# Kernel tuning notes

Hardware: AMD Instinct MI355X
Metric: run time of the kernel (lower is better)

Reference implementation:

```python
import jax, jax.numpy as jnp
import numpy as np

N_QUBITS = 4
LAYERS = 2
NUM_HEADS = 8
EMBED = 32
DK = EMBED // NUM_HEADS  # == N_QUBITS
B, S = 32, 4096


def _ry(t):
    c, s = jnp.cos(t / 2), jnp.sin(t / 2)
    m = jnp.stack([jnp.stack([c, -s], -1), jnp.stack([s, c], -1)], -2)
    return m.astype(jnp.complex64)


def _rx(t):
    c = jnp.cos(t / 2).astype(jnp.complex64)
    s = (-1j) * jnp.sin(t / 2).astype(jnp.complex64)
    return jnp.stack([jnp.stack([c, s], -1), jnp.stack([s, c], -1)], -2)


def _rz(t):
    em = jnp.exp(-0.5j * t.astype(jnp.complex64))
    ep = jnp.conj(em)
    z = jnp.zeros_like(em)
    return jnp.stack([jnp.stack([em, z], -1), jnp.stack([z, ep], -1)], -2)


def _apply_1q(state, U, w, n):
    # state: (B, 2**n); wire 0 is the most-significant bit (PennyLane convention)
    s = state.reshape(-1, 2 ** w, 2, 2 ** (n - 1 - w))
    if U.ndim == 2:  # shared gate
        s = jnp.einsum('ij,bpjq->bpiq', U, s)
    else:  # per-token gate, U: (B,2,2)
        s = jnp.einsum('bij,bpjq->bpiq', U, s)
    return s.reshape(-1, 2 ** n)


def _cnot(state, c, t, n):
    s = state.reshape((-1,) + (2,) * n)
    c_ax, t_ax = 1 + c, 1 + t
    s0 = jax.lax.slice_in_dim(s, 0, 1, axis=c_ax)
    s1 = jax.lax.slice_in_dim(s, 1, 2, axis=c_ax)
    s1 = jnp.flip(s1, axis=t_ax)  # X on target where control == 1
    s = jnp.concatenate([s0, s1], axis=c_ax)
    return s.reshape(-1, 2 ** n)


def _z_expvals(state, n):
    p = jnp.abs(state) ** 2  # (B, 2**n)
    outs = []
    for i in range(n):
        pr = p.reshape(-1, 2 ** i, 2, 2 ** (n - 1 - i))
        outs.append(pr[:, :, 0, :].sum((1, 2)) - pr[:, :, 1, :].sum((1, 2)))
    return jnp.stack(outs, -1)  # (B, n)


def _head_fwd(x_h, p_h):
    # x_h: (BT, n_qubits) angles, p_h: (layers, n_qubits, 3)
    n, L = N_QUBITS, LAYERS
    bt = x_h.shape[0]
    state = jnp.zeros((bt, 2 ** n), jnp.complex64).at[:, 0].set(1.0)
    for i in range(n):
        state = _apply_1q(state, _ry(x_h[:, i]), i, n)
    for l in range(L):
        for i in range(n):
            state = _apply_1q(state, _rx(p_h[l, i, 0]), i, n)
            state = _apply_1q(state, _ry(p_h[l, i, 1]), i, n)
            state = _apply_1q(state, _rz(p_h[l, i, 2]), i, n)
        for i in range(n - 1):
            state = _cnot(state, i, i + 1, n)
        state = _cnot(state, n - 1, 0, n)
    return _z_expvals(state, n)


def setup_inputs() -> dict:
    key = jax.random.key(0)
    k1, k2, k3, k4 = jax.random.split(key, 4)
    x = jax.random.normal(k1, (B, S, EMBED), jnp.float32)
    params = jax.random.normal(k2, (NUM_HEADS, LAYERS, N_QUBITS, 3), jnp.float32)
    fan_in = NUM_HEADS * N_QUBITS
    bound = 1.0 / np.sqrt(fan_in)
    W_out = jax.random.uniform(k3, (EMBED, fan_in), jnp.float32, -bound, bound)
    b_out = jax.random.uniform(k4, (EMBED,), jnp.float32, -bound, bound)
    return {'x': x, 'params': params, 'W_out': W_out, 'b_out': b_out}


def reference(x, params, W_out, b_out):
    b, s, e = x.shape
    xh = x.reshape(b, s, NUM_HEADS, DK)
    xh = jnp.moveaxis(xh, 2, 0).reshape(NUM_HEADS, b * s, DK)  # (H, BT, d_k)
    ang = xh[:, :, :N_QUBITS]  # angles fed into RY embedding
    ev = jax.vmap(_head_fwd)(ang, params)  # (H, BT, n_qubits)
    concat = jnp.moveaxis(ev, 0, 1).reshape(b, s, NUM_HEADS * N_QUBITS)
    return concat @ W_out.T + b_out
```

## Files before the change

kernel.cpp:

```cpp
#include <hip/hip_runtime.h>
#include <math.h>

#define NQ   4
#define NH   8
#define NL   2
#define DIM  16
#define EMB  32
#define TPB  64

__global__ void build_unitaries_kernel(const float* __restrict__ params,
                                       float* __restrict__ Uws) {
    int tid = threadIdx.x;
    int h   = tid >> 4;
    int col = tid & 15;

    float re[DIM], im[DIM];
#pragma unroll
    for (int j = 0; j < DIM; ++j) { re[j] = (j == col) ? 1.f : 0.f; im[j] = 0.f; }

#pragma unroll
    for (int l = 0; l < NL; ++l) {
#pragma unroll
        for (int q = 0; q < NQ; ++q) {
            const float* p = params + ((h * NL + l) * NQ + q) * 3;
            const int m = 1 << (3 - q);
            {
                float s, c; __sincosf(0.5f * p[0], &s, &c);
#pragma unroll
                for (int j = 0; j < DIM; ++j) {
                    if (j & m) continue;
                    const int j1 = j | m;
                    float r0 = re[j], i0 = im[j], r1 = re[j1], i1 = im[j1];
                    re[j]  = c * r0 + s * i1;
                    im[j]  = c * i0 - s * r1;
                    re[j1] = s * i0 + c * r1;
                    im[j1] = -s * r0 + c * i1;
                }
            }
            {
                float s, c; __sincosf(0.5f * p[1], &s, &c);
#pragma unroll
                for (int j = 0; j < DIM; ++j) {
                    if (j & m) continue;
                    const int j1 = j | m;
                    float r0 = re[j], i0 = im[j], r1 = re[j1], i1 = im[j1];
                    re[j]  = c * r0 - s * r1;
                    im[j]  = c * i0 - s * i1;
                    re[j1] = s * r0 + c * r1;
                    im[j1] = s * i0 + c * i1;
                }
            }
            {
                float s, c; __sincosf(0.5f * p[2], &s, &c);
#pragma unroll
                for (int j = 0; j < DIM; ++j) {
                    if (j & m) continue;
                    const int j1 = j | m;
                    float r0 = re[j], i0 = im[j], r1 = re[j1], i1 = im[j1];
                    re[j]  = c * r0 + s * i0;
                    im[j]  = c * i0 - s * r0;
                    re[j1] = c * r1 - s * i1;
                    im[j1] = c * i1 + s * r1;
                }
            }
        }
#pragma unroll
        for (int e = 0; e < NQ; ++e) {
            const int cm = 1 << (3 - e), tm = 1 << (3 - ((e + 1) & 3));
#pragma unroll
            for (int j = 0; j < DIM; ++j) {
                if ((j & cm) && !(j & tm)) {
                    const int j1 = j | tm;
                    float tr = re[j]; re[j] = re[j1]; re[j1] = tr;
                    float ti = im[j]; im[j] = im[j1]; im[j1] = ti;
                }
            }
        }
    }
#pragma unroll
    for (int j = 0; j < DIM; ++j) {
        Uws[(h * DIM + j) * DIM + col]        = re[j];
        Uws[2048 + (h * DIM + j) * DIM + col] = im[j];
    }
}

__global__ __launch_bounds__(512, 4)
void qmha_kernel(const float* __restrict__ x,
                 const float* __restrict__ Uws,
                 const float* __restrict__ W,
                 const float* __restrict__ bvec,
                 float* __restrict__ out,
                 int ntok) {
    __shared__ float evs[EMB * TPB];
    __shared__ float Wt[EMB * 36];

    const int tid  = threadIdx.x;
    const int tok0 = blockIdx.x * TPB;

    {
        const int idx = tid * 2;
        const float2 w2 = *(const float2*)(W + idx);
        const int e0 = idx >> 5, k0 = idx & 31;
        const int e1 = (idx + 1) >> 5, k1 = (idx + 1) & 31;
        Wt[k0 * 36 + e0] = w2.x;
        Wt[k1 * 36 + e1] = w2.y;
    }

    {
        int h = __builtin_amdgcn_readfirstlane(tid >> 6);
        const int t = tid & 63;
        const int tok = tok0 + t;
        if (tok < ntok) {
            const float4 xa = *(const float4*)(x + (size_t)tok * EMB + h * NQ);
            float c0, s0, c1, s1, c2, s2, c3, s3;
            __sincosf(0.5f * xa.x, &s0, &c0);
            __sincosf(0.5f * xa.y, &s1, &c1);
            __sincosf(0.5f * xa.z, &s2, &c2);
            __sincosf(0.5f * xa.w, &s3, &c3);

            float p01[4], p23[4], a[DIM];
            p01[0] = c0 * c1; p01[1] = c0 * s1; p01[2] = s0 * c1; p01[3] = s0 * s1;
            p23[0] = c2 * c3; p23[1] = c2 * s3; p23[2] = s2 * c3; p23[3] = s2 * s3;
#pragma unroll
            for (int j = 0; j < DIM; ++j) a[j] = p01[j >> 2] * p23[j & 3];

            const float* Ur = Uws + h * 256;
            const float* Ui = Uws + 2048 + h * 256;

            float ev0 = 0.f, ev1 = 0.f, ev2 = 0.f, ev3 = 0.f;
#pragma unroll
            for (int j = 0; j < DIM; ++j) {
                float ar = 0.f, ai = 0.f;
#pragma unroll
                for (int k = 0; k < DIM; ++k) {
                    ar = fmaf(Ur[j * DIM + k], a[k], ar);
                    ai = fmaf(Ui[j * DIM + k], a[k], ai);
                }
                const float pj = ar * ar + ai * ai;
                ev0 += (j & 8) ? -pj : pj;
                ev1 += (j & 4) ? -pj : pj;
                ev2 += (j & 2) ? -pj : pj;
                ev3 += (j & 1) ? -pj : pj;
            }

            evs[(h * 4 + 0) * TPB + t] = ev0;
            evs[(h * 4 + 1) * TPB + t] = ev1;
            evs[(h * 4 + 2) * TPB + t] = ev2;
            evs[(h * 4 + 3) * TPB + t] = ev3;
        }
    }
    __syncthreads();

    {
        const int t2 = tid >> 3;
        const int eg = tid & 7;
        const int tok = tok0 + t2;
        if (tok < ntok) {
            const float4 bv = *(const float4*)(bvec + eg * 4);
            float o0 = bv.x, o1 = bv.y, o2 = bv.z, o3 = bv.w;
#pragma unroll
            for (int k = 0; k < EMB; ++k) {
                const float evk = evs[k * TPB + t2];
                const float4 wk = *(const float4*)(Wt + k * 36 + eg * 4);
                o0 = fmaf(wk.x, evk, o0);
                o1 = fmaf(wk.y, evk, o1);
                o2 = fmaf(wk.z, evk, o2);
                o3 = fmaf(wk.w, evk, o3);
            }
            float4 v; v.x = o0; v.y = o1; v.z = o2; v.w = o3;
            *(float4*)(out + (size_t)tok * EMB + eg * 4) = v;
        }
    }
}

extern "C" void kernel_launch(void* const* d_in, const int* in_sizes, int n_in,
                              void* d_out, int out_size, void* d_ws, size_t ws_size,
                              hipStream_t stream) {
    const float* x      = (const float*)d_in[0];
    const float* params = (const float*)d_in[1];
    const float* W_out  = (const float*)d_in[2];
    const float* b_out  = (const float*)d_in[3];
    float*       out    = (float*)d_out;
    float*       Uws    = (float*)d_ws;

    const int ntok = in_sizes[0] / EMB;

    hipLaunchKernelGGL(build_unitaries_kernel, dim3(1), dim3(128), 0, stream,
                       params, Uws);

    const int blocks = (ntok + TPB - 1) / TPB;
    hipLaunchKernelGGL(qmha_kernel, dim3(blocks), dim3(512), 0, stream,
                       x, Uws, W_out, b_out, out, ntok);
}
```

Measured before the change: 93.88 us.

## Compute per-head unitary-state product with split-fp16 MFMA instead of scalar FMAs

```diff
diff --git a/kernel.cpp b/kernel.cpp
--- a/kernel.cpp
+++ b/kernel.cpp
@@ -7,6 +7,12 @@
 #define DIM  16
 #define EMB  32
 #define TPB  64
+
+#define LO_SCALE 4096.0f
+#define LO_INV   (1.0f/4096.0f)
+
+typedef _Float16 f16x8  __attribute__((ext_vector_type(8)));
+typedef float    f32x16 __attribute__((ext_vector_type(16)));
 
 __global__ void build_unitaries_kernel(const float* __restrict__ params,
                                        float* __restrict__ Uws) {
@@ -77,10 +83,28 @@
             }
         }
     }
+
+    _Float16* Ah = (_Float16*)Uws;
+    _Float16* Al = Ah + 4096;
+    const int khigh = col >> 3, e = col & 7;
 #pragma unroll
     for (int j = 0; j < DIM; ++j) {
-        Uws[(h * DIM + j) * DIM + col]        = re[j];
-        Uws[2048 + (h * DIM + j) * DIM + col] = im[j];
+        {
+            const float v = re[j];
+            const _Float16 h16 = (_Float16)v;
+            const float lo = (v - (float)h16) * LO_SCALE;
+            const int lane = j + 32 * khigh;
+            Ah[(h * 64 + lane) * 8 + e] = h16;
+            Al[(h * 64 + lane) * 8 + e] = (_Float16)lo;
+        }
+        {
+            const float v = im[j];
+            const _Float16 h16 = (_Float16)v;
+            const float lo = (v - (float)h16) * LO_SCALE;
+            const int lane = 16 + j + 32 * khigh;
+            Ah[(h * 64 + lane) * 8 + e] = h16;
+            Al[(h * 64 + lane) * 8 + e] = (_Float16)lo;
+        }
     }
 }
 
@@ -107,46 +131,76 @@
     }
 
     {
-        int h = __builtin_amdgcn_readfirstlane(tid >> 6);
-        const int t = tid & 63;
-        const int tok = tok0 + t;
-        if (tok < ntok) {
-            const float4 xa = *(const float4*)(x + (size_t)tok * EMB + h * NQ);
+        const int h    = tid >> 6;
+        const int lane = tid & 63;
+        const int lh   = lane & 31;
+        const int hi   = lane >> 5;
+
+        const _Float16* Ah = (const _Float16*)Uws;
+        const _Float16* Al = Ah + 4096;
+        const f16x8 Afh = *(const f16x8*)(Ah + (h * 64 + lane) * 8);
+        const f16x8 Afl = *(const f16x8*)(Al + (h * 64 + lane) * 8);
+
+#pragma unroll
+        for (int g = 0; g < 2; ++g) {
+            const int t    = g * 32 + lh;
+            const int tok  = tok0 + t;
+            const int tokc = (tok < ntok) ? tok : (ntok - 1);
+
+            const float4 xa = *(const float4*)(x + (size_t)tokc * EMB + h * NQ);
             float c0, s0, c1, s1, c2, s2, c3, s3;
             __sincosf(0.5f * xa.x, &s0, &c0);
             __sincosf(0.5f * xa.y, &s1, &c1);
             __sincosf(0.5f * xa.z, &s2, &c2);
             __sincosf(0.5f * xa.w, &s3, &c3);
 
-            float p01[4], p23[4], a[DIM];
-            p01[0] = c0 * c1; p01[1] = c0 * s1; p01[2] = s0 * c1; p01[3] = s0 * s1;
-            p23[0] = c2 * c3; p23[1] = c2 * s3; p23[2] = s2 * c3; p23[3] = s2 * s3;
-#pragma unroll
-            for (int j = 0; j < DIM; ++j) a[j] = p01[j >> 2] * p23[j & 3];
-
-            const float* Ur = Uws + h * 256;
-            const float* Ui = Uws + 2048 + h * 256;
-
-            float ev0 = 0.f, ev1 = 0.f, ev2 = 0.f, ev3 = 0.f;
-#pragma unroll
-            for (int j = 0; j < DIM; ++j) {
-                float ar = 0.f, ai = 0.f;
-#pragma unroll
-                for (int k = 0; k < DIM; ++k) {
-                    ar = fmaf(Ur[j * DIM + k], a[k], ar);
-                    ai = fmaf(Ui[j * DIM + k], a[k], ai);
-                }
-                const float pj = ar * ar + ai * ai;
-                ev0 += (j & 8) ? -pj : pj;
-                ev1 += (j & 4) ? -pj : pj;
-                ev2 += (j & 2) ? -pj : pj;
-                ev3 += (j & 1) ? -pj : pj;
-            }
-
-            evs[(h * 4 + 0) * TPB + t] = ev0;
-            evs[(h * 4 + 1) * TPB + t] = ev1;
-            evs[(h * 4 + 2) * TPB + t] = ev2;
-            evs[(h * 4 + 3) * TPB + t] = ev3;
+            const float f  = hi ? s0 : c0;
+            const float pA = f * c1, pB = f * s1;
+            const float p23[4] = {c2 * c3, c2 * s3, s2 * c3, s2 * s3};
+
+            f16x8 bh, bl;
+#pragma unroll
+            for (int e = 0; e < 8; ++e) {
+                const float av = ((e >> 2) ? pB : pA) * p23[e & 3];
+                const _Float16 ah16 = (_Float16)av;
+                bh[e] = ah16;
+                bl[e] = (_Float16)((av - (float)ah16) * LO_SCALE);
+            }
+
+            f32x16 accH, accL;
+#pragma unroll
+            for (int i = 0; i < 16; ++i) { accH[i] = 0.f; accL[i] = 0.f; }
+            accH = __builtin_amdgcn_mfma_f32_32x32x16_f16(Afh, bh, accH, 0, 0, 0);
+            accL = __builtin_amdgcn_mfma_f32_32x32x16_f16(Afl, bh, accL, 0, 0, 0);
+            accL = __builtin_amdgcn_mfma_f32_32x32x16_f16(Afh, bl, accL, 0, 0, 0);
+
+            float pj[8];
+#pragma unroll
+            for (int r = 0; r < 8; ++r) {
+                const float ar = fmaf(accL[r],     LO_INV, accH[r]);
+                const float ai = fmaf(accL[r + 8], LO_INV, accH[r + 8]);
+                pj[r] = ar * ar + ai * ai;
+            }
+            const float s01 = pj[0] + pj[1], s23 = pj[2] + pj[3];
+            const float s45 = pj[4] + pj[5], s67 = pj[6] + pj[7];
+            const float sa = s01 + s23, sb = s45 + s67;
+            float ev0 = sa - sb;
+            const float tot = sa + sb;
+            float ev1 = hi ? -tot : tot;
+            float ev2 = (s01 + s45) - (s23 + s67);
+            float ev3 = (pj[0] - pj[1]) + (pj[2] - pj[3]) +
+                        (pj[4] - pj[5]) + (pj[6] - pj[7]);
+            ev0 += __shfl_xor(ev0, 32);
+            ev1 += __shfl_xor(ev1, 32);
+            ev2 += __shfl_xor(ev2, 32);
+            ev3 += __shfl_xor(ev3, 32);
+
+            if (hi == 0 && tok < ntok) {
+                evs[(h * 4 + 0) * TPB + t] = ev0;
+                evs[(h * 4 + 1) * TPB + t] = ev1;
+                evs[(h * 4 + 2) * TPB + t] = ev2;
+                evs[(h * 4 + 3) * TPB + t] = ev3;
+            }
         }
     }
     __syncthreads();
```

New measurement: 87.17 us. 7.1% less time.
